# Kernel tuning notes

Measured on AMD Instinct MI355X. Metric: run time of the kernel, lower is better.

## Reference

```python
import jax, jax.numpy as jnp
import numpy as np
from jax import lax

B, T, C = 512, 128, 66
H, L, W = 512, 2, 10


def gru_cell(x, h, W_ih, W_hh, b_ih, b_hh):
    # PyTorch GRU gate order: r, z, n
    gi = x @ W_ih.T + b_ih            # [B, 3H]
    gh = h @ W_hh.T + b_hh            # [B, 3H]
    i_r, i_z, i_n = jnp.split(gi, 3, axis=-1)
    h_r, h_z, h_n = jnp.split(gh, 3, axis=-1)
    r = jax.nn.sigmoid(i_r + h_r)
    z = jax.nn.sigmoid(i_z + h_z)
    n = jnp.tanh(i_n + r * h_n)
    return (1.0 - z) * n + z * h


def setup_inputs() -> dict:
    key = jax.random.key(0)
    ks = jax.random.split(key, 16)
    s = 0.02
    inp = {
        "x": jax.random.normal(ks[0], (B, T, C), jnp.float32),
        # GRU layer 0 (input C -> hidden H)
        "W_ih0": jax.random.normal(ks[1], (3 * H, C), jnp.float32) * s,
        "W_hh0": jax.random.normal(ks[2], (3 * H, H), jnp.float32) * s,
        "b_ih0": jnp.zeros((3 * H,), jnp.float32),
        "b_hh0": jnp.zeros((3 * H,), jnp.float32),
        # GRU layer 1 (hidden H -> hidden H)
        "W_ih1": jax.random.normal(ks[3], (3 * H, H), jnp.float32) * s,
        "W_hh1": jax.random.normal(ks[4], (3 * H, H), jnp.float32) * s,
        "b_ih1": jnp.zeros((3 * H,), jnp.float32),
        "b_hh1": jnp.zeros((3 * H,), jnp.float32),
        # temporal_fc: Linear(window_size, 1) -> weight [1, W], bias [1]
        "temporal_w": jax.random.normal(ks[5], (1, W), jnp.float32) * s,
        "temporal_b": jnp.zeros((1,), jnp.float32),
        # spatial_fc: Linear(H, C)
        "spatial_w": jax.random.normal(ks[6], (C, H), jnp.float32) * s,
        "spatial_b": jnp.zeros((C,), jnp.float32),
    }
    return inp


def _forward(x, W_ih0, W_hh0, b_ih0, b_hh0, W_ih1, W_hh1, b_ih1, b_hh1,
             temporal_w, temporal_b, spatial_w, spatial_b):
    p0 = (W_ih0, W_hh0, b_ih0, b_hh0)
    p1 = (W_ih1, W_hh1, b_ih1, b_hh1)

    # ---- encoder: 2-layer GRU over the full sequence ----
    xs = jnp.transpose(x, (1, 0, 2))  # [T, B, C]
    h0 = jnp.zeros((x.shape[0], H), x.dtype)

    def make_step(p):
        def step(h, xt):
            hn = gru_cell(xt, h, *p)
            return hn, hn
        return step

    hT0, ys0 = lax.scan(make_step(p0), h0, xs)          # ys0 [T,B,H]
    hT1, ys1 = lax.scan(make_step(p1), h0, ys0)         # ys1 [T,B,H]

    encoder_window = jnp.transpose(ys1[-W:], (1, 0, 2))  # [B, W, H]
    last_input_frame = x[:, -1, :]                       # [B, C]

    def dec_step(carry, _):
        (h_0, h_1), win, dec_in = carry
        h_0n = gru_cell(dec_in, h_0, *p0)
        h_1n = gru_cell(h_0n, h_1, *p1)                  # decoder_out [B,H]
        win = jnp.concatenate([win[:, 1:, :], h_1n[:, None, :]], axis=1)
        # temporal_fc over window axis: [B,W,H] -> [B,H]
        t = jnp.einsum('bwh,w->bh', win, temporal_w[0]) + temporal_b[0]
        frame = t @ spatial_w.T + spatial_b + dec_in     # recursive residual
        return ((h_0n, h_1n), win, frame), frame

    init = ((hT0, hT1), encoder_window, last_input_frame)
    _, frames = lax.scan(dec_step, init, None, length=T)  # [T,B,C]
    return jnp.transpose(frames, (1, 0, 2))               # [B,T,C]


def reference(x, W_ih0, W_hh0, b_ih0, b_hh0, W_ih1, W_hh1, b_ih1, b_hh1,
              temporal_w, temporal_b, spatial_w, spatial_b):
    return _forward(x, W_ih0, W_hh0, b_ih0, b_hh0, W_ih1, W_hh1, b_ih1, b_hh1,
                    temporal_w, temporal_b, spatial_w, spatial_b)
```

## Files before the change

kernel.cpp:

```cpp
#include <hip/hip_runtime.h>
#include <hip/hip_bf16.h>

typedef __attribute__((ext_vector_type(8))) short bf16x8;
typedef __attribute__((ext_vector_type(4))) float f32x4;

#define NB 512
#define NT 128
#define NC 66
#define NH 512
#define NW 10
#define CP 96
#define BM 32
#define BJ 64
#define NWG 256
#define NTHR 256
#define G3 1536
#define NKS_H 16
#define NKS_X 3

struct Params {
  const float *x, *Wih0, *Whh0, *bih0, *bhh0, *Wih1, *Whh1, *bih1, *bhh1, *tw, *tb, *sw, *sb;
  float *out;
  unsigned *barL, *barG;
  __hip_bfloat16 *Wih0h, *Wih0l;
  __hip_bfloat16 *Wch, *Wcl;
  __hip_bfloat16 *Whh0H, *Whh0L;
  __hip_bfloat16 *Wih1H, *Wih1L;
  __hip_bfloat16 *Whh1H, *Whh1L;
  float *cb;
  float *h0, *h1, *tvec;
  __hip_bfloat16 *winb;
};

__device__ __forceinline__ float sigmoidf_(float x) { return 1.f / (1.f + __expf(-x)); }
__device__ __forceinline__ float tanhf_(float x) {
  float e = __expf(2.f * x);
  return (e - 1.f) / (e + 1.f);
}
__device__ __forceinline__ void split2(float v, __hip_bfloat16& h, __hip_bfloat16& l) {
  h = __float2bfloat16(v);
  l = __float2bfloat16(v - __bfloat162float(h));
}
__device__ __forceinline__ unsigned short bfbits(__hip_bfloat16 h) { return *(unsigned short*)&h; }
__device__ __forceinline__ void splitpack4(float4 v, ushort4& ph, ushort4& pl) {
  __hip_bfloat16 h, l;
  split2(v.x, h, l); ph.x = bfbits(h); pl.x = bfbits(l);
  split2(v.y, h, l); ph.y = bfbits(h); pl.y = bfbits(l);
  split2(v.z, h, l); ph.z = bfbits(h); pl.z = bfbits(l);
  split2(v.w, h, l); ph.w = bfbits(h); pl.w = bfbits(l);
}

__device__ __forceinline__ float4 cload4(const float* p) {
  unsigned long long a = __hip_atomic_load((const unsigned long long*)p,       __ATOMIC_RELAXED, __HIP_MEMORY_SCOPE_AGENT);
  unsigned long long b = __hip_atomic_load(((const unsigned long long*)p) + 1, __ATOMIC_RELAXED, __HIP_MEMORY_SCOPE_AGENT);
  float4 r;
  ((unsigned long long*)&r)[0] = a;
  ((unsigned long long*)&r)[1] = b;
  return r;
}

__device__ __forceinline__ void gbar(unsigned* barL, unsigned* barG, unsigned& phase,
                                     int tid, int grp) {
  __syncthreads();
  ++phase;
  if (tid == 0) {
    unsigned old = __hip_atomic_fetch_add(&barL[grp * 32], 1u, __ATOMIC_RELEASE,
                                          __HIP_MEMORY_SCOPE_AGENT);
    if (old == phase * 32 - 1)
      __hip_atomic_fetch_add(barG, 1u, __ATOMIC_RELAXED, __HIP_MEMORY_SCOPE_AGENT);
    while (__hip_atomic_load(barG, __ATOMIC_RELAXED, __HIP_MEMORY_SCOPE_AGENT) < phase)
      __builtin_amdgcn_s_sleep(2);
  }
  __syncthreads();
  asm volatile("" ::: "memory");
}

#define AM_X 0
#define AM_H 2

__device__ __forceinline__ void zacc(f32x4 acc[2][4]) {
#pragma unroll
  for (int i = 0; i < 2; ++i)
#pragma unroll
    for (int g = 0; g < 4; ++g) {
      acc[i][g][0] = 0.f; acc[i][g][1] = 0.f; acc[i][g][2] = 0.f; acc[i][g][3] = 0.f;
    }
}

template <int G2, int AMODE>
__device__ __forceinline__ void gemm_frag(
    f32x4 acc[2][4],
    const __hip_bfloat16* __restrict__ WH, const __hip_bfloat16* __restrict__ WL,
    const int nks,
    const float* __restrict__ A, int tstep, int b0, int j0, int tid)
{
  const int wv = tid >> 6, lane = tid & 63, quad = lane >> 4, l15 = lane & 15;
  const int ms = wv & 1, jh = wv >> 1;
  const int arow = b0 + ms * 16 + l15;

  unsigned boff[6];
#pragma unroll
  for (int c = 0; c < 3; ++c)
#pragma unroll
    for (int jl = 0; jl < 2; ++jl) {
      const int jb = c * 32 + (j0 >> 4) + jh * 2 + jl;
      boff[c * 2 + jl] = (unsigned)((jb * nks) * 64 + lane) * 8u;
    }

  const float* arp = (AMODE == AM_X)
      ? A + ((size_t)arow * NT + tstep) * NC
      : A + (size_t)arow * NH + (quad << 3);

  uint4 bh0[6], bl0[6], bh1[6], bl1[6];
  float a0[8], a1[8];

  auto loadB = [&](uint4 (&bh)[6], uint4 (&bl)[6], int st) {
    const unsigned so = (unsigned)st * 512u;
#pragma unroll
    for (int f = 0; f < 6; ++f) {
      bh[f] = *(const uint4*)(WH + boff[f] + so);
      bl[f] = *(const uint4*)(WL + boff[f] + so);
    }
  };
  auto loadAfr = [&](float (&a)[8], int st) {
    if (AMODE == AM_X) {
      const int k0 = st * 32 + (quad << 3);
#pragma unroll
      for (int e = 0; e < 8; ++e) a[e] = (k0 + e < NC) ? arp[k0 + e] : 0.f;
    } else {
      const float4 v0 = cload4(arp + st * 32);
      const float4 v1 = cload4(arp + st * 32 + 4);
      a[0] = v0.x; a[1] = v0.y; a[2] = v0.z; a[3] = v0.w;
      a[4] = v1.x; a[5] = v1.y; a[6] = v1.z; a[7] = v1.w;
    }
  };
  auto comp = [&](const uint4 (&bh)[6], const uint4 (&bl)[6], const float (&a)[8]) {
    float4 v0, v1;
    v0.x = a[0]; v0.y = a[1]; v0.z = a[2]; v0.w = a[3];
    v1.x = a[4]; v1.y = a[5]; v1.z = a[6]; v1.w = a[7];
    ushort4 ph0, pl0, ph1, pl1;
    splitpack4(v0, ph0, pl0);
    splitpack4(v1, ph1, pl1);
    bf16x8 ah, al;
    ((ushort4*)&ah)[0] = ph0; ((ushort4*)&ah)[1] = ph1;
    ((ushort4*)&al)[0] = pl0; ((ushort4*)&al)[1] = pl1;
#pragma unroll
    for (int jl = 0; jl < 2; ++jl)
#pragma unroll
      for (int c = 0; c < 3; ++c) {
        const int f = c * 2 + jl;
        const int g = (c == 2) ? G2 : c;
        const bf16x8 vbh = *(const bf16x8*)&bh[f];
        const bf16x8 vbl = *(const bf16x8*)&bl[f];
        acc[jl][g] = __builtin_amdgcn_mfma_f32_16x16x32_bf16(ah, vbh, acc[jl][g], 0, 0, 0);
        acc[jl][g] = __builtin_amdgcn_mfma_f32_16x16x32_bf16(al, vbh, acc[jl][g], 0, 0, 0);
        acc[jl][g] = __builtin_amdgcn_mfma_f32_16x16x32_bf16(ah, vbl, acc[jl][g], 0, 0, 0);
      }
  };

  loadB(bh0, bl0, 0);
  loadAfr(a0, 0);
  if (nks > 1) { loadB(bh1, bl1, 1); loadAfr(a1, 1); }
  for (int st = 0; st < nks; st += 2) {
    comp(bh0, bl0, a0);
    if (st + 2 < nks) { loadB(bh0, bl0, st + 2); loadAfr(a0, st + 2); }
    if (st + 1 < nks) {
      comp(bh1, bl1, a1);
      if (st + 3 < nks) { loadB(bh1, bl1, st + 3); loadAfr(a1, st + 3); }
    }
  }
}

__device__ __forceinline__ void ew_gru(
    f32x4 acc[2][4],
    const float* __restrict__ bi, const float* __restrict__ bh,
    const float* __restrict__ hold, float* __restrict__ hnew,
    int b0, int j0, int tid, __hip_bfloat16* win, int slot)
{
  const int wv = tid >> 6, lane = tid & 63, quad = lane >> 4, l15 = lane & 15;
  const int ms = wv & 1, jh = wv >> 1;
#pragma unroll
  for (int jlf = 0; jlf < 2; ++jlf) {
    const int j = j0 + jh * 32 + jlf * 16 + l15;
    const float br = bi[j] + bh[j];
    const float bz = bi[NH + j] + bh[NH + j];
    const float bni = bi[2 * NH + j];
    const float bnh = bh[2 * NH + j];
#pragma unroll
    for (int rg = 0; rg < 4; ++rg) {
      const int b = b0 + ms * 16 + quad * 4 + rg;
      const float r = sigmoidf_(acc[jlf][0][rg] + br);
      const float z = sigmoidf_(acc[jlf][1][rg] + bz);
      const float n = tanhf_(acc[jlf][2][rg] + bni + r * (acc[jlf][3][rg] + bnh));
      const float h = hold[(size_t)b * NH + j];
      const float hn = (1.f - z) * n + z * h;
      hnew[(size_t)b * NH + j] = hn;
      if (win) win[((size_t)b * NW + slot) * NH + j] = __float2bfloat16(hn);
    }
  }
}

__device__ __forceinline__ void ew_dec1(
    f32x4 acc[2][4], const Params& P, float* __restrict__ h1p,
    int b0, int j0, int tid, int s)
{
  const int wv = tid >> 6, lane = tid & 63, quad = lane >> 4, l15 = lane & 15;
  const int ms = wv & 1, jh = wv >> 1;
  const int slot = s % NW;
  float twv[NW];
#pragma unroll
  for (int k = 0; k < NW; ++k) {
    int idx = k - slot - 1; if (idx < 0) idx += NW;
    twv[k] = P.tw[idx];
  }
  const float tw9 = P.tw[NW - 1];
  const float tb0 = P.tb[0];
#pragma unroll
  for (int jlf = 0; jlf < 2; ++jlf) {
    const int j = j0 + jh * 32 + jlf * 16 + l15;
    const float br = P.bih1[j] + P.bhh1[j];
    const float bz = P.bih1[NH + j] + P.bhh1[NH + j];
    const float bni = P.bih1[2 * NH + j];
    const float bnh = P.bhh1[2 * NH + j];
#pragma unroll
    for (int rg = 0; rg < 4; ++rg) {
      const int b = b0 + ms * 16 + quad * 4 + rg;
      const float r = sigmoidf_(acc[jlf][0][rg] + br);
      const float z = sigmoidf_(acc[jlf][1][rg] + bz);
      const float n = tanhf_(acc[jlf][2][rg] + bni + r * (acc[jlf][3][rg] + bnh));
      const float h = h1p[(size_t)b * NH + j];
      const float hn = (1.f - z) * n + z * h;
      h1p[(size_t)b * NH + j] = hn;
      __hip_bfloat16* wrow = P.winb + (size_t)b * NW * NH + j;
      wrow[(size_t)slot * NH] = __float2bfloat16(hn);
      float ts = tb0 + hn * tw9;
#pragma unroll
      for (int k = 0; k < NW; ++k) {
        if (k == slot) continue;
        ts += __bfloat162float(wrow[(size_t)k * NH]) * twv[k];
      }
      P.tvec[(size_t)b * NH + j] = ts;
    }
  }
}

__global__ __launch_bounds__(NTHR) void rnn_kernel(Params P) {
  __shared__ __align__(16) float tl[4 * NH];
  const int tid = threadIdx.x;
  const int wg = blockIdx.x;
  const int grp = wg & 7;
  const size_t gid = (size_t)wg * NTHR + tid;
  const size_t GT = (size_t)NWG * NTHR;
  unsigned phase = 0;
  const int wv = tid >> 6, lane = tid & 63, l15 = lane & 15;
  const int jh = wv >> 1;

  for (size_t f = gid; f < (size_t)G3 * CP / 8; f += GT) {
    const int ln = (int)(f & 63), blk = (int)(f >> 6);
    const int ks = blk % NKS_X, jb = blk / NKS_X;
    const int r = jb * 16 + (ln & 15);
    const int k0 = ks * 32 + ((ln >> 4) << 3);
#pragma unroll
    for (int e = 0; e < 8; ++e) {
      const int k = k0 + e;
      split2(k < NC ? P.Wih0[(size_t)r * NC + k] : 0.f,
             P.Wih0h[f * 8 + e], P.Wih0l[f * 8 + e]);
    }
  }
  {
    const float* srcs[3] = { P.Whh0, P.Wih1, P.Whh1 };
    __hip_bfloat16* dhs[3] = { P.Whh0H, P.Wih1H, P.Whh1H };
    __hip_bfloat16* dls[3] = { P.Whh0L, P.Wih1L, P.Whh1L };
#pragma unroll
    for (int m = 0; m < 3; ++m) {
      const float* __restrict__ W = srcs[m];
      __hip_bfloat16* __restrict__ DH = dhs[m];
      __hip_bfloat16* __restrict__ DL = dls[m];
      for (size_t f = gid; f < (size_t)G3 * NH / 8; f += GT) {
        const int ln = (int)(f & 63), blk = (int)(f >> 6);
        const int ks = blk & 15, jb = blk >> 4;
        const int r = jb * 16 + (ln & 15);
        const int k0 = ks * 32 + ((ln >> 4) << 3);
        const float* src = W + (size_t)r * NH + k0;
        ushort4 h0v, l0v, h1v, l1v;
        splitpack4(*(const float4*)(src), h0v, l0v);
        splitpack4(*(const float4*)(src + 4), h1v, l1v);
        *(ushort4*)(DH + f * 8)     = h0v;
        *(ushort4*)(DH + f * 8 + 4) = h1v;
        *(ushort4*)(DL + f * 8)     = l0v;
        *(ushort4*)(DL + f * 8 + 4) = l1v;
      }
    }
  }
  for (size_t f = gid; f < (size_t)G3 * NH / 8; f += GT) {
    const int ln = (int)(f & 63), blk = (int)(f >> 6);
    const int ks = blk & 15, jb = blk >> 4;
    const int r = jb * 16 + (ln & 15);
    const int k0 = ks * 32 + ((ln >> 4) << 3);
    float s[8] = {0.f, 0.f, 0.f, 0.f, 0.f, 0.f, 0.f, 0.f};
    for (int c = 0; c < NC; ++c) {
      const float a = P.Wih0[(size_t)r * NC + c];
      const float4 w0 = *(const float4*)(P.sw + (size_t)c * NH + k0);
      const float4 w1 = *(const float4*)(P.sw + (size_t)c * NH + k0 + 4);
      s[0] += a * w0.x; s[1] += a * w0.y; s[2] += a * w0.z; s[3] += a * w0.w;
      s[4] += a * w1.x; s[5] += a * w1.y; s[6] += a * w1.z; s[7] += a * w1.w;
    }
#pragma unroll
    for (int e = 0; e < 8; ++e) split2(s[e], P.Wch[f * 8 + e], P.Wcl[f * 8 + e]);
  }
  for (size_t i = gid; i < (size_t)G3; i += GT) {
    float a = 0.f;
    for (int c = 0; c < NC; ++c) a += P.Wih0[i * NC + c] * P.sb[c];
    P.cb[i] = a;
  }
  for (size_t i = gid; i < (size_t)2 * NB * NH; i += GT) { P.h0[i] = 0.f; P.h1[i] = 0.f; }
  gbar(P.barL, P.barG, phase, tid, grp);

  const bool isL1 = wg >= 128;
  const int tile = wg & 127;
  const int b0 = (tile >> 3) * BM;
  const int j0 = (tile & 7) * BJ;

  float G[2][3][4];

  for (int t = 0; t <= NT; ++t) {
    const int cur = t & 1;
    float* h0c = P.h0 + (size_t)cur * NB * NH;
    float* h0n = P.h0 + (size_t)(cur ^ 1) * NB * NH;
    float* h1c = P.h1 + (size_t)cur * NB * NH;
    float* h1n = P.h1 + (size_t)(cur ^ 1) * NB * NH;
    f32x4 acc[2][4];
    if (!isL1) {
      if (t < NT) {
        zacc(acc);
        gemm_frag<2, AM_X>(acc, P.Wih0h, P.Wih0l, NKS_X, P.x, t, b0, j0, tid);
        gemm_frag<3, AM_H>(acc, P.Whh0H, P.Whh0L, NKS_H, h0c, 0, b0, j0, tid);
        ew_gru(acc, P.bih0, P.bhh0, h0c, h0n, b0, j0, tid, nullptr, 0);
      } else {
        zacc(acc);
        gemm_frag<2, AM_X>(acc, P.Wih0h, P.Wih0l, NKS_X, P.x, NT - 1, b0, j0, tid);
#pragma unroll
        for (int jlf = 0; jlf < 2; ++jlf)
#pragma unroll
          for (int c = 0; c < 3; ++c)
#pragma unroll
            for (int rg = 0; rg < 4; ++rg) G[jlf][c][rg] = acc[jlf][c][rg];
      }
    } else {
      if (t >= 1) {
        zacc(acc);
        gemm_frag<2, AM_H>(acc, P.Wih1H, P.Wih1L, NKS_H, h0c, 0, b0, j0, tid);
        gemm_frag<3, AM_H>(acc, P.Whh1H, P.Whh1L, NKS_H, h1c, 0, b0, j0, tid);
        ew_gru(acc, P.bih1, P.bhh1, h1c, h1n, b0, j0, tid,
               (t >= 119) ? P.winb : nullptr, t - 119);
      }
    }
    gbar(P.barL, P.barG, phase, tid, grp);
  }

  int d0 = 0;
  float* h1p = P.h1 + (size_t)NB * NH;

  float cbr[2][3];
  float Freg[2];
  if (!isL1) {
#pragma unroll
    for (int jlf = 0; jlf < 2; ++jlf)
#pragma unroll
      for (int c = 0; c < 3; ++c)
        cbr[jlf][c] = P.cb[c * NH + j0 + jh * 32 + jlf * 16 + l15];
#pragma unroll
    for (int v = 0; v < 2; ++v) {
      const int t2 = tid + v * NTHR;
      if (t2 < 4 * NC) {
        const int bl = t2 / NC, c = t2 - bl * NC, b = wg * 4 + bl;
        Freg[v] = P.x[((size_t)b * NT + (NT - 1)) * NC + c];
      }
    }
  }

  auto frame_out = [&](int sout) {
    const float* tvb = P.tvec + (size_t)wg * 4 * NH;
    *(float4*)&tl[tid * 8] = cload4(tvb + tid * 8);
    *(float4*)&tl[tid * 8 + 4] = cload4(tvb + tid * 8 + 4);
    __syncthreads();
#pragma unroll
    for (int v = 0; v < 2; ++v) {
      const int t2 = tid + v * NTHR;
      if (t2 < 4 * NC) {
        const int bl = t2 / NC, c = t2 - bl * NC, b = wg * 4 + bl;
        float f = Freg[v] + P.sb[c];
        const float4* swr = (const float4*)(P.sw + (size_t)c * NH);
        const float4* tr = (const float4*)(tl + bl * NH);
#pragma unroll 8
        for (int h4 = 0; h4 < NH / 4; ++h4) {
          float4 tv = tr[h4], wv4 = swr[h4];
          f += tv.x * wv4.x + tv.y * wv4.y + tv.z * wv4.z + tv.w * wv4.w;
        }
        Freg[v] = f;
        P.out[((size_t)b * NT + sout) * NC + c] = f;
      }
    }
    __syncthreads();
  };

  for (int s = 0; s < NT; ++s) {
    float* h0c = P.h0 + (size_t)d0 * NB * NH;
    float* h0n = P.h0 + (size_t)(d0 ^ 1) * NB * NH;
    f32x4 acc[2][4];
    if (!isL1) {
      if (s >= 1) frame_out(s - 1);
      zacc(acc);
      if (s >= 1)
        gemm_frag<2, AM_H>(acc, P.Wch, P.Wcl, NKS_H, P.tvec, 0, b0, j0, tid);
#pragma unroll
      for (int jlf = 0; jlf < 2; ++jlf)
#pragma unroll
        for (int c = 0; c < 3; ++c)
#pragma unroll
          for (int rg = 0; rg < 4; ++rg) {
            float g = G[jlf][c][rg] + acc[jlf][c][rg] + (s >= 1 ? cbr[jlf][c] : 0.f);
            G[jlf][c][rg] = g;
            acc[jlf][c][rg] = g;
          }
      gemm_frag<3, AM_H>(acc, P.Whh0H, P.Whh0L, NKS_H, h0c, 0, b0, j0, tid);
      ew_gru(acc, P.bih0, P.bhh0, h0c, h0n, b0, j0, tid, nullptr, 0);
    } else {
      zacc(acc);
      gemm_frag<3, AM_H>(acc, P.Whh1H, P.Whh1L, NKS_H, h1p, 0, b0, j0, tid);
    }
    gbar(P.barL, P.barG, phase, tid, grp);
    if (isL1) {
      gemm_frag<2, AM_H>(acc, P.Wih1H, P.Wih1L, NKS_H, h0n, 0, b0, j0, tid);
      ew_dec1(acc, P, h1p, b0, j0, tid, s);
    }
    gbar(P.barL, P.barG, phase, tid, grp);
    d0 ^= 1;
  }
  if (!isL1) frame_out(NT - 1);
}

extern "C" void kernel_launch(void* const* d_in, const int* in_sizes, int n_in,
                              void* d_out, int out_size, void* d_ws, size_t ws_size,
                              hipStream_t stream) {
  (void)in_sizes; (void)n_in; (void)out_size; (void)ws_size;
  Params P;
  P.x    = (const float*)d_in[0];
  P.Wih0 = (const float*)d_in[1];
  P.Whh0 = (const float*)d_in[2];
  P.bih0 = (const float*)d_in[3];
  P.bhh0 = (const float*)d_in[4];
  P.Wih1 = (const float*)d_in[5];
  P.Whh1 = (const float*)d_in[6];
  P.bih1 = (const float*)d_in[7];
  P.bhh1 = (const float*)d_in[8];
  P.tw   = (const float*)d_in[9];
  P.tb   = (const float*)d_in[10];
  P.sw   = (const float*)d_in[11];
  P.sb   = (const float*)d_in[12];
  P.out  = (float*)d_out;

  char* w = (char*)d_ws;
  size_t used = 0;
  auto take = [&](size_t bytes) {
    char* p = w + used;
    used += (bytes + 255) & ~(size_t)255;
    return p;
  };
  unsigned* bar = (unsigned*)take(2048);
  P.barL = bar;
  P.barG = bar + 8 * 32;
  P.Wih0h = (__hip_bfloat16*)take((size_t)G3 * CP * 2);
  P.Wih0l = (__hip_bfloat16*)take((size_t)G3 * CP * 2);
  P.Wch   = (__hip_bfloat16*)take((size_t)G3 * NH * 2);
  P.Wcl   = (__hip_bfloat16*)take((size_t)G3 * NH * 2);
  P.Whh0H = (__hip_bfloat16*)take((size_t)G3 * NH * 2);
  P.Whh0L = (__hip_bfloat16*)take((size_t)G3 * NH * 2);
  P.Wih1H = (__hip_bfloat16*)take((size_t)G3 * NH * 2);
  P.Wih1L = (__hip_bfloat16*)take((size_t)G3 * NH * 2);
  P.Whh1H = (__hip_bfloat16*)take((size_t)G3 * NH * 2);
  P.Whh1L = (__hip_bfloat16*)take((size_t)G3 * NH * 2);
  P.cb    = (float*)take((size_t)G3 * 4);
  P.h0    = (float*)take((size_t)2 * NB * NH * 4);
  P.h1    = (float*)take((size_t)2 * NB * NH * 4);
  P.tvec  = (float*)take((size_t)NB * NH * 4);
  P.winb  = (__hip_bfloat16*)take((size_t)NB * NW * NH * 2);

  hipMemsetAsync(d_ws, 0, 2048, stream);
  rnn_kernel<<<dim3(NWG), dim3(NTHR), 0, stream>>>(P);
}
```

Baseline: 14.62 ms.

## Store hidden states pre-split in MFMA fragment layout and stage A via LDS

Hidden states and the temporal vector are also written in a pre-split bf16 hi/lo packed, swizzled fragment layout when produced. Each GEMM then bulk-loads its 32-row A tile into LDS with coalesced 64-bit atomic loads and reads fragments from there. This replaces the per-step scattered fp32 global loads and the repeated hi/lo splitting of A in every wave. The cost is extra global writes per element, 128KB of LDS per workgroup (lower occupancy), and extra __syncthreads.

```diff
diff --git a/kernel.cpp b/kernel.cpp
--- a/kernel.cpp
+++ b/kernel.cpp
@@ -3,6 +3,7 @@
 
 typedef __attribute__((ext_vector_type(8))) short bf16x8;
 typedef __attribute__((ext_vector_type(4))) float f32x4;
+typedef unsigned long long ull;
 
 #define NB 512
 #define NT 128
@@ -17,6 +18,7 @@
 #define G3 1536
 #define NKS_H 16
 #define NKS_X 3
+#define FRAGN (NB * NH)
 
 struct Params {
   const float *x, *Wih0, *Whh0, *bih0, *bhh0, *Wih1, *Whh1, *bih1, *bhh1, *tw, *tb, *sw, *sb;
@@ -29,6 +31,7 @@
   __hip_bfloat16 *Whh1H, *Whh1L;
   float *cb;
   float *h0, *h1, *tvec;
+  unsigned *h0f, *h1f, *tvf;
   __hip_bfloat16 *winb;
 };
 
@@ -49,13 +52,22 @@
   split2(v.z, h, l); ph.z = bfbits(h); pl.z = bfbits(l);
   split2(v.w, h, l); ph.w = bfbits(h); pl.w = bfbits(l);
 }
+__device__ __forceinline__ unsigned packbf(float v) {
+  __hip_bfloat16 h, l; split2(v, h, l);
+  return (unsigned)bfbits(h) | ((unsigned)bfbits(l) << 16);
+}
+__device__ __forceinline__ unsigned fragidx(int b, int j) {
+  const int lanep = (b & 15) | (((j >> 3) & 3) << 4);
+  const unsigned s = ((unsigned)(lanep * 8 + (j & 7))) ^ ((unsigned)(lanep & 7) << 2);
+  return ((unsigned)((b >> 4) * 16 + (j >> 5))) * 512u + s;
+}
 
 __device__ __forceinline__ float4 cload4(const float* p) {
-  unsigned long long a = __hip_atomic_load((const unsigned long long*)p,       __ATOMIC_RELAXED, __HIP_MEMORY_SCOPE_AGENT);
-  unsigned long long b = __hip_atomic_load(((const unsigned long long*)p) + 1, __ATOMIC_RELAXED, __HIP_MEMORY_SCOPE_AGENT);
+  ull a = __hip_atomic_load((const ull*)p,       __ATOMIC_RELAXED, __HIP_MEMORY_SCOPE_AGENT);
+  ull b = __hip_atomic_load(((const ull*)p) + 1, __ATOMIC_RELAXED, __HIP_MEMORY_SCOPE_AGENT);
   float4 r;
-  ((unsigned long long*)&r)[0] = a;
-  ((unsigned long long*)&r)[1] = b;
+  ((ull*)&r)[0] = a;
+  ((ull*)&r)[1] = b;
   return r;
 }
 
@@ -75,9 +87,6 @@
   asm volatile("" ::: "memory");
 }
 
-#define AM_X 0
-#define AM_H 2
-
 __device__ __forceinline__ void zacc(f32x4 acc[2][4]) {
 #pragma unroll
   for (int i = 0; i < 2; ++i)
@@ -87,16 +96,27 @@
     }
 }
 
-template <int G2, int AMODE>
-__device__ __forceinline__ void gemm_frag(
+__device__ __forceinline__ void bulk_a(unsigned* __restrict__ alds,
+                                       const unsigned* __restrict__ frag,
+                                       int bb0, int tid) {
+  const ull* g = (const ull*)(frag + (size_t)bb0 * 8192);
+  ull* d = (ull*)alds;
+  ull v[32];
+#pragma unroll
+  for (int i = 0; i < 32; ++i)
+    v[i] = __hip_atomic_load(g + i * 256 + tid, __ATOMIC_RELAXED, __HIP_MEMORY_SCOPE_AGENT);
+#pragma unroll
+  for (int i = 0; i < 32; ++i) d[i * 256 + tid] = v[i];
+}
+
+template <int G2>
+__device__ __forceinline__ void gemm_lds(
     f32x4 acc[2][4],
     const __hip_bfloat16* __restrict__ WH, const __hip_bfloat16* __restrict__ WL,
-    const int nks,
-    const float* __restrict__ A, int tstep, int b0, int j0, int tid)
+    const unsigned* __restrict__ aT, int j0, int tid)
 {
-  const int wv = tid >> 6, lane = tid & 63, quad = lane >> 4, l15 = lane & 15;
+  const int wv = tid >> 6, lane = tid & 63;
   const int ms = wv & 1, jh = wv >> 1;
-  const int arow = b0 + ms * 16 + l15;
 
   unsigned boff[6];
 #pragma unroll
@@ -104,16 +124,12 @@
 #pragma unroll
     for (int jl = 0; jl < 2; ++jl) {
       const int jb = c * 32 + (j0 >> 4) + jh * 2 + jl;
-      boff[c * 2 + jl] = (unsigned)((jb * nks) * 64 + lane) * 8u;
-    }
-
-  const float* arp = (AMODE == AM_X)
-      ? A + ((size_t)arow * NT + tstep) * NC
-      : A + (size_t)arow * NH + (quad << 3);
+      boff[c * 2 + jl] = (unsigned)((jb * NKS_H) * 64 + lane) * 8u;
+    }
+  const unsigned* ab = aT + ms * 8192;
+  const unsigned i0 = ((unsigned)(lane * 8)) ^ ((unsigned)(lane & 7) << 2);
 
   uint4 bh0[6], bl0[6], bh1[6], bl1[6];
-  float a0[8], a1[8];
-
   auto loadB = [&](uint4 (&bh)[6], uint4 (&bl)[6], int st) {
     const unsigned so = (unsigned)st * 512u;
 #pragma unroll
@@ -122,28 +138,19 @@
       bl[f] = *(const uint4*)(WL + boff[f] + so);
     }
   };
-  auto loadAfr = [&](float (&a)[8], int st) {
-    if (AMODE == AM_X) {
-      const int k0 = st * 32 + (quad << 3);
-#pragma unroll
-      for (int e = 0; e < 8; ++e) a[e] = (k0 + e < NC) ? arp[k0 + e] : 0.f;
-    } else {
-      const float4 v0 = cload4(arp + st * 32);
-      const float4 v1 = cload4(arp + st * 32 + 4);
-      a[0] = v0.x; a[1] = v0.y; a[2] = v0.z; a[3] = v0.w;
-      a[4] = v1.x; a[5] = v1.y; a[6] = v1.z; a[7] = v1.w;
-    }
-  };
-  auto comp = [&](const uint4 (&bh)[6], const uint4 (&bl)[6], const float (&a)[8]) {
-    float4 v0, v1;
-    v0.x = a[0]; v0.y = a[1]; v0.z = a[2]; v0.w = a[3];
-    v1.x = a[4]; v1.y = a[5]; v1.z = a[6]; v1.w = a[7];
-    ushort4 ph0, pl0, ph1, pl1;
-    splitpack4(v0, ph0, pl0);
-    splitpack4(v1, ph1, pl1);
-    bf16x8 ah, al;
-    ((ushort4*)&ah)[0] = ph0; ((ushort4*)&ah)[1] = ph1;
-    ((ushort4*)&al)[0] = pl0; ((ushort4*)&al)[1] = pl1;
+  auto readA = [&](bf16x8& ah, bf16x8& al, int st) {
+    const unsigned* ap = ab + st * 512;
+    const uint4 ua = *(const uint4*)(ap + i0);
+    const uint4 ub = *(const uint4*)(ap + (i0 ^ 4u));
+    uint4 uh, ul;
+    uh.x = (ua.x & 0xffffu) | (ua.y << 16);  ul.x = (ua.x >> 16) | (ua.y & 0xffff0000u);
+    uh.y = (ua.z & 0xffffu) | (ua.w << 16);  ul.y = (ua.z >> 16) | (ua.w & 0xffff0000u);
+    uh.z = (ub.x & 0xffffu) | (ub.y << 16);  ul.z = (ub.x >> 16) | (ub.y & 0xffff0000u);
+    uh.w = (ub.z & 0xffffu) | (ub.w << 16);  ul.w = (ub.z >> 16) | (ub.w & 0xffff0000u);
+    ah = *(const bf16x8*)&uh;
+    al = *(const bf16x8*)&ul;
+  };
+  auto comp = [&](const uint4 (&bh)[6], const uint4 (&bl)[6], bf16x8 ah, bf16x8 al) {
 #pragma unroll
     for (int jl = 0; jl < 2; ++jl)
 #pragma unroll
@@ -158,23 +165,90 @@
       }
   };
 
-  loadB(bh0, bl0, 0);
-  loadAfr(a0, 0);
-  if (nks > 1) { loadB(bh1, bl1, 1); loadAfr(a1, 1); }
-  for (int st = 0; st < nks; st += 2) {
-    comp(bh0, bl0, a0);
-    if (st + 2 < nks) { loadB(bh0, bl0, st + 2); loadAfr(a0, st + 2); }
-    if (st + 1 < nks) {
-      comp(bh1, bl1, a1);
-      if (st + 3 < nks) { loadB(bh1, bl1, st + 3); loadAfr(a1, st + 3); }
-    }
-  }
+  bf16x8 a0h, a0l, a1h, a1l;
+  loadB(bh0, bl0, 0); loadB(bh1, bl1, 1);
+  readA(a0h, a0l, 0); readA(a1h, a1l, 1);
+  for (int st = 0; st < NKS_H; st += 2) {
+    comp(bh0, bl0, a0h, a0l);
+    if (st + 2 < NKS_H) { loadB(bh0, bl0, st + 2); readA(a0h, a0l, st + 2); }
+    comp(bh1, bl1, a1h, a1l);
+    if (st + 3 < NKS_H) { loadB(bh1, bl1, st + 3); readA(a1h, a1l, st + 3); }
+  }
+}
+
+template <int G2>
+__device__ __forceinline__ void gemm_x(
+    f32x4 acc[2][4],
+    const __hip_bfloat16* __restrict__ WH, const __hip_bfloat16* __restrict__ WL,
+    const float* __restrict__ X, int tstep, int b0, int j0, int tid)
+{
+  const int wv = tid >> 6, lane = tid & 63, quad = lane >> 4, l15 = lane & 15;
+  const int ms = wv & 1, jh = wv >> 1;
+  const int arow = b0 + ms * 16 + l15;
+
+  unsigned boff[6];
+#pragma unroll
+  for (int c = 0; c < 3; ++c)
+#pragma unroll
+    for (int jl = 0; jl < 2; ++jl) {
+      const int jb = c * 32 + (j0 >> 4) + jh * 2 + jl;
+      boff[c * 2 + jl] = (unsigned)((jb * NKS_X) * 64 + lane) * 8u;
+    }
+  const float* arp = X + ((size_t)arow * NT + tstep) * NC;
+
+  float a[3][8];
+#pragma unroll
+  for (int st = 0; st < 3; ++st) {
+    const int k0 = st * 32 + (quad << 3);
+#pragma unroll
+    for (int e = 0; e < 8; ++e) a[st][e] = (k0 + e < NC) ? arp[k0 + e] : 0.f;
+  }
+
+  uint4 bh0[6], bl0[6], bh1[6], bl1[6];
+  auto loadB = [&](uint4 (&bh)[6], uint4 (&bl)[6], int st) {
+    const unsigned so = (unsigned)st * 512u;
+#pragma unroll
+    for (int f = 0; f < 6; ++f) {
+      bh[f] = *(const uint4*)(WH + boff[f] + so);
+      bl[f] = *(const uint4*)(WL + boff[f] + so);
+    }
+  };
+  auto comp = [&](const uint4 (&bh)[6], const uint4 (&bl)[6], const float (&av)[8]) {
+    float4 v0, v1;
+    v0.x = av[0]; v0.y = av[1]; v0.z = av[2]; v0.w = av[3];
+    v1.x = av[4]; v1.y = av[5]; v1.z = av[6]; v1.w = av[7];
+    ushort4 ph0, pl0, ph1, pl1;
+    splitpack4(v0, ph0, pl0);
+    splitpack4(v1, ph1, pl1);
+    bf16x8 ah, al;
+    ((ushort4*)&ah)[0] = ph0; ((ushort4*)&ah)[1] = ph1;
+    ((ushort4*)&al)[0] = pl0; ((ushort4*)&al)[1] = pl1;
+#pragma unroll
+    for (int jl = 0; jl < 2; ++jl)
+#pragma unroll
+      for (int c = 0; c < 3; ++c) {
+        const int f = c * 2 + jl;
+        const int g = (c == 2) ? G2 : c;
+        const bf16x8 vbh = *(const bf16x8*)&bh[f];
+        const bf16x8 vbl = *(const bf16x8*)&bl[f];
+        acc[jl][g] = __builtin_amdgcn_mfma_f32_16x16x32_bf16(ah, vbh, acc[jl][g], 0, 0, 0);
+        acc[jl][g] = __builtin_amdgcn_mfma_f32_16x16x32_bf16(al, vbh, acc[jl][g], 0, 0, 0);
+        acc[jl][g] = __builtin_amdgcn_mfma_f32_16x16x32_bf16(ah, vbl, acc[jl][g], 0, 0, 0);
+      }
+  };
+
+  loadB(bh0, bl0, 0); loadB(bh1, bl1, 1);
+  comp(bh0, bl0, a[0]);
+  loadB(bh0, bl0, 2);
+  comp(bh1, bl1, a[1]);
+  comp(bh0, bl0, a[2]);
 }
 
 __device__ __forceinline__ void ew_gru(
     f32x4 acc[2][4],
     const float* __restrict__ bi, const float* __restrict__ bh,
     const float* __restrict__ hold, float* __restrict__ hnew,
+    unsigned* __restrict__ hfrag,
     int b0, int j0, int tid, __hip_bfloat16* win, int slot)
 {
   const int wv = tid >> 6, lane = tid & 63, quad = lane >> 4, l15 = lane & 15;
@@ -195,6 +269,7 @@
       const float h = hold[(size_t)b * NH + j];
       const float hn = (1.f - z) * n + z * h;
       hnew[(size_t)b * NH + j] = hn;
+      hfrag[fragidx(b, j)] = packbf(hn);
       if (win) win[((size_t)b * NW + slot) * NH + j] = __float2bfloat16(hn);
     }
   }
@@ -231,6 +306,7 @@
       const float h = h1p[(size_t)b * NH + j];
       const float hn = (1.f - z) * n + z * h;
       h1p[(size_t)b * NH + j] = hn;
+      P.h1f[FRAGN + fragidx(b, j)] = packbf(hn);
       __hip_bfloat16* wrow = P.winb + (size_t)b * NW * NH + j;
       wrow[(size_t)slot * NH] = __float2bfloat16(hn);
       float ts = tb0 + hn * tw9;
@@ -240,11 +316,14 @@
         ts += __bfloat162float(wrow[(size_t)k * NH]) * twv[k];
       }
       P.tvec[(size_t)b * NH + j] = ts;
+      P.tvf[fragidx(b, j)] = packbf(ts);
     }
   }
 }
 
 __global__ __launch_bounds__(NTHR) void rnn_kernel(Params P) {
+  __shared__ __align__(16) unsigned aT0[16384];
+  __shared__ __align__(16) unsigned aT1[16384];
   __shared__ __align__(16) float tl[4 * NH];
   const int tid = threadIdx.x;
   const int wg = blockIdx.x;
@@ -314,12 +393,15 @@
     P.cb[i] = a;
   }
   for (size_t i = gid; i < (size_t)2 * NB * NH; i += GT) { P.h0[i] = 0.f; P.h1[i] = 0.f; }
+  for (size_t i = gid; i < (size_t)2 * FRAGN; i += GT) { P.h0f[i] = 0u; P.h1f[i] = 0u; }
+  for (size_t i = gid; i < (size_t)FRAGN; i += GT) P.tvf[i] = 0u;
   gbar(P.barL, P.barG, phase, tid, grp);
 
   const bool isL1 = wg >= 128;
   const int tile = wg & 127;
   const int b0 = (tile >> 3) * BM;
   const int j0 = (tile & 7) * BJ;
+  const int bb0 = b0 >> 4;
 
   float G[2][3][4];
 
@@ -333,12 +415,15 @@
     if (!isL1) {
       if (t < NT) {
         zacc(acc);
-        gemm_frag<2, AM_X>(acc, P.Wih0h, P.Wih0l, NKS_X, P.x, t, b0, j0, tid);
-        gemm_frag<3, AM_H>(acc, P.Whh0H, P.Whh0L, NKS_H, h0c, 0, b0, j0, tid);
-        ew_gru(acc, P.bih0, P.bhh0, h0c, h0n, b0, j0, tid, nullptr, 0);
+        bulk_a(aT0, P.h0f + (size_t)cur * FRAGN, bb0, tid);
+        gemm_x<2>(acc, P.Wih0h, P.Wih0l, P.x, t, b0, j0, tid);
+        __syncthreads();
+        gemm_lds<3>(acc, P.Whh0H, P.Whh0L, aT0, j0, tid);
+        ew_gru(acc, P.bih0, P.bhh0, h0c, h0n, P.h0f + (size_t)(cur ^ 1) * FRAGN,
+               b0, j0, tid, nullptr, 0);
       } else {
         zacc(acc);
-        gemm_frag<2, AM_X>(acc, P.Wih0h, P.Wih0l, NKS_X, P.x, NT - 1, b0, j0, tid);
+        gemm_x<2>(acc, P.Wih0h, P.Wih0l, P.x, NT - 1, b0, j0, tid);
 #pragma unroll
         for (int jlf = 0; jlf < 2; ++jlf)
 #pragma unroll
@@ -349,10 +434,13 @@
     } else {
       if (t >= 1) {
         zacc(acc);
-        gemm_frag<2, AM_H>(acc, P.Wih1H, P.Wih1L, NKS_H, h0c, 0, b0, j0, tid);
-        gemm_frag<3, AM_H>(acc, P.Whh1H, P.Whh1L, NKS_H, h1c, 0, b0, j0, tid);
-        ew_gru(acc, P.bih1, P.bhh1, h1c, h1n, b0, j0, tid,
-               (t >= 119) ? P.winb : nullptr, t - 119);
+        bulk_a(aT0, P.h0f + (size_t)cur * FRAGN, bb0, tid);
+        bulk_a(aT1, P.h1f + (size_t)cur * FRAGN, bb0, tid);
+        __syncthreads();
+        gemm_lds<2>(acc, P.Wih1H, P.Wih1L, aT0, j0, tid);
+        gemm_lds<3>(acc, P.Whh1H, P.Whh1L, aT1, j0, tid);
+        ew_gru(acc, P.bih1, P.bhh1, h1c, h1n, P.h1f + (size_t)(cur ^ 1) * FRAGN,
+               b0, j0, tid, (t >= 119) ? P.winb : nullptr, t - 119);
       }
     }
     gbar(P.barL, P.barG, phase, tid, grp);
@@ -411,8 +499,11 @@
     if (!isL1) {
       if (s >= 1) frame_out(s - 1);
       zacc(acc);
+      bulk_a(aT1, P.h0f + (size_t)d0 * FRAGN, bb0, tid);
+      if (s >= 1) bulk_a(aT0, P.tvf, bb0, tid);
+      __syncthreads();
       if (s >= 1)
-        gemm_frag<2, AM_H>(acc, P.Wch, P.Wcl, NKS_H, P.tvec, 0, b0, j0, tid);
+        gemm_lds<2>(acc, P.Wch, P.Wcl, aT0, j0, tid);
 #pragma unroll
       for (int jlf = 0; jlf < 2; ++jlf)
 #pragma unroll
@@ -423,15 +514,20 @@
             G[jlf][c][rg] = g;
             acc[jlf][c][rg] = g;
           }
-      gemm_frag<3, AM_H>(acc, P.Whh0H, P.Whh0L, NKS_H, h0c, 0, b0, j0, tid);
-      ew_gru(acc, P.bih0, P.bhh0, h0c, h0n, b0, j0, tid, nullptr, 0);
+      gemm_lds<3>(acc, P.Whh0H, P.Whh0L, aT1, j0, tid);
+      ew_gru(acc, P.bih0, P.bhh0, h0c, h0n, P.h0f + (size_t)(d0 ^ 1) * FRAGN,
+             b0, j0, tid, nullptr, 0);
     } else {
       zacc(acc);
-      gemm_frag<3, AM_H>(acc, P.Whh1H, P.Whh1L, NKS_H, h1p, 0, b0, j0, tid);
+      bulk_a(aT0, P.h1f + (size_t)FRAGN, bb0, tid);
+      __syncthreads();
+      gemm_lds<3>(acc, P.Whh1H, P.Whh1L, aT0, j0, tid);
     }
     gbar(P.barL, P.barG, phase, tid, grp);
     if (isL1) {
-      gemm_frag<2, AM_H>(acc, P.Wih1H, P.Wih1L, NKS_H, h0n, 0, b0, j0, tid);
+      bulk_a(aT1, P.h0f + (size_t)(d0 ^ 1) * FRAGN, bb0, tid);
+      __syncthreads();
+      gemm_lds<2>(acc, P.Wih1H, P.Wih1L, aT1, j0, tid);
       ew_dec1(acc, P, h1p, b0, j0, tid, s);
     }
     gbar(P.barL, P.barG, phase, tid, grp);
@@ -484,6 +580,9 @@
   P.h0    = (float*)take((size_t)2 * NB * NH * 4);
   P.h1    = (float*)take((size_t)2 * NB * NH * 4);
   P.tvec  = (float*)take((size_t)NB * NH * 4);
+  P.h0f   = (unsigned*)take((size_t)2 * FRAGN * 4);
+  P.h1f   = (unsigned*)take((size_t)2 * FRAGN * 4);
+  P.tvf   = (unsigned*)take((size_t)FRAGN * 4);
   P.winb  = (__hip_bfloat16*)take((size_t)NB * NW * NH * 2);
 
   hipMemsetAsync(d_ws, 0, 2048, stream);
```

Result: slower. 39.75 ms (+171.9%).
